# Optimization experiments

Measured on AMD Instinct MI355X. Metric: run time of the kernel, lower is better.

The kernel has to match this reference:

```python
import jax, jax.numpy as jnp
import numpy as np

B, N, M = 2, 2048, 2048
D = 1024          # query_dim == context_dim == inner_dim
H, DH = 16, 64    # heads, dim_head
SCALE = DH ** -0.5


def setup_inputs() -> dict:
    key = jax.random.key(0)
    ks = jax.random.split(key, 7)
    s = 0.02
    return {
        "x": jax.random.normal(ks[0], (B, N, D), jnp.float32),
        "context": jax.random.normal(ks[1], (B, M, D), jnp.float32),
        "Wq": jax.random.normal(ks[2], (D, H * DH), jnp.float32) * s,
        "Wk": jax.random.normal(ks[3], (D, H * DH), jnp.float32) * s,
        "Wv": jax.random.normal(ks[4], (D, H * DH), jnp.float32) * s,
        "Wo": jax.random.normal(ks[5], (H * DH, D), jnp.float32) * s,
        "bo": jax.random.normal(ks[6], (D,), jnp.float32) * s,
    }


def reference(x, context, Wq, Wk, Wv, Wo, bo):
    # Linear projections (bias-free, as in to_q/to_k/to_v)
    q = (x @ Wq).reshape(B, N, H, DH)        # [B,N,H,DH]
    k = (context @ Wk).reshape(B, M, H, DH)  # [B,M,H,DH]
    v = (context @ Wv).reshape(B, M, H, DH)
    # QK^T * scale, softmax over keys, then AV
    sim = jnp.einsum('bnhd,bmhd->bhnm', q, k) * SCALE  # [B,H,N,M]
    attn = jax.nn.softmax(sim, axis=-1)
    out = jnp.einsum('bhnm,bmhd->bnhd', attn, v)       # [B,N,H,DH]
    out = out.reshape(B, N, H * DH)
    return out @ Wo + bo  # to_out Linear; dropout=0 is identity
```

## Files before the change

### kernel.cpp

```cpp
#include <hip/hip_runtime.h>

#define B_  2
#define N_  2048
#define M_  2048
#define D_  1024
#define H_  16
#define DH_ 64

typedef __bf16 bf16x8 __attribute__((ext_vector_type(8)));
typedef __bf16 bf16x4 __attribute__((ext_vector_type(4)));
typedef short  short4v __attribute__((ext_vector_type(4)));
typedef float  f32x4  __attribute__((ext_vector_type(4)));
typedef unsigned int u32x4v __attribute__((ext_vector_type(4)));

#define GAS(p) ((__attribute__((address_space(1))) void*)(p))
#define LAS(p) ((__attribute__((address_space(3))) void*)(p))

#define QPRESCALE 0.18033688011112042f

__device__ __forceinline__ unsigned short f2bf(float f) {
    unsigned int u = __builtin_bit_cast(unsigned int, f);
    u += 0x7fffu + ((u >> 16) & 1u);
    return (unsigned short)(u >> 16);
}

__device__ __forceinline__ unsigned cvtpkbf(float a, float b) {
    unsigned r;
    asm("v_cvt_pk_bf16_f32 %0, %1, %2" : "=v"(r) : "v"(a), "v"(b));
    return r;
}

__global__ __launch_bounds__(256) void prep(
    const float* __restrict__ x, const float* __restrict__ ctx,
    const float* __restrict__ Wq, const float* __restrict__ Wk,
    const float* __restrict__ Wv, const float* __restrict__ Wo,
    unsigned short* __restrict__ xb, unsigned short* __restrict__ cb,
    unsigned short* __restrict__ WTbase)
{
    if (blockIdx.z == 4) {
        int blk = blockIdx.y * 32 + blockIdx.x;
        int stride = 1024 * 256;
        for (int i = blk * 256 + threadIdx.x; i < 2097152; i += stride) {
            const float4* src; unsigned short* dst; int j;
            if (i < 1048576) { src = (const float4*)x;   dst = xb; j = i; }
            else             { src = (const float4*)ctx; dst = cb; j = i - 1048576; }
            float4 v = src[j];
            ushort4 o = make_ushort4(f2bf(v.x), f2bf(v.y), f2bf(v.z), f2bf(v.w));
            *(ushort4*)(dst + 4*j) = o;
        }
        return;
    }
    const float* W = (blockIdx.z == 0) ? Wq : (blockIdx.z == 1) ? Wk
                    : (blockIdx.z == 2) ? Wv : Wo;
    unsigned short* WT = WTbase + (size_t)blockIdx.z * 1048576;
    __shared__ unsigned short t[32][33];
    int tx = threadIdx.x & 31, ty8 = threadIdx.x >> 5;
    int c = blockIdx.x * 32 + tx;
#pragma unroll
    for (int i = 0; i < 4; ++i) {
        int r = blockIdx.y * 32 + i*8 + ty8;
        t[i*8 + ty8][tx] = f2bf(W[(size_t)r * 1024 + c]);
    }
    __syncthreads();
    int c2 = blockIdx.y * 32 + tx;
#pragma unroll
    for (int i = 0; i < 4; ++i) {
        int r2 = blockIdx.x * 32 + i*8 + ty8;
        WT[(size_t)r2 * 1024 + c2] = t[tx][i*8 + ty8];
    }
}

__global__ __launch_bounds__(256) void gemm128(
    const unsigned short* __restrict__ xb,
    const unsigned short* __restrict__ cb,
    const unsigned short* __restrict__ wT,
    const unsigned short* __restrict__ aoA,
    unsigned short* __restrict__ qkv_out,
    const float* __restrict__ bo,
    float* __restrict__ outF,
    int base_mode)
{
    __shared__ __align__(16) unsigned short As[128*32];
    __shared__ __align__(16) unsigned short Bs[128*32];

    const int mode = base_mode + blockIdx.z;
    const unsigned short* Amat;
    const unsigned short* Bt;
    if (mode == 0)      { Amat = wT;               Bt = xb; }
    else if (mode == 1) { Amat = wT + 1048576;     Bt = cb; }
    else if (mode == 2) { Amat = cb;               Bt = wT + 2*1048576; }
    else                { Amat = wT + 3*1048576;   Bt = aoA; }

    const int tid = threadIdx.x;
    const int w = tid >> 6, l = tid & 63;
    const int quad = l >> 4, l16 = l & 15;
    const int wm = w & 1, wn = w >> 1;
    int row0, col0;
    if (mode == 2) { row0 = blockIdx.x * 128; col0 = blockIdx.y * 128; }
    else           { row0 = blockIdx.y * 128; col0 = blockIdx.x * 128; }

    f32x4 acc[4][4];
#pragma unroll
    for (int i = 0; i < 4; ++i)
#pragma unroll
        for (int j = 0; j < 4; ++j) acc[i][j] = (f32x4){0.f, 0.f, 0.f, 0.f};

    for (int k0 = 0; k0 < 1024; k0 += 32) {
        __syncthreads();
#pragma unroll
        for (int i = 0; i < 2; ++i) {
            int s = i*256 + w*64 + l;
            int m = s >> 2, c = s & 3;
            int cs = c ^ ((m >> 1) & 3);
            __builtin_amdgcn_global_load_lds(
                GAS(Amat + (size_t)(row0 + m)*1024 + k0 + cs*8),
                LAS(As + (i*256 + w*64)*8), 16, 0, 0);
            __builtin_amdgcn_global_load_lds(
                GAS(Bt + (size_t)(col0 + m)*1024 + k0 + cs*8),
                LAS(Bs + (i*256 + w*64)*8), 16, 0, 0);
        }
        __syncthreads();

        bf16x8 af[4], bfr[4];
#pragma unroll
        for (int mt = 0; mt < 4; ++mt) {
            int m = wm*64 + mt*16 + l16;
            af[mt] = *reinterpret_cast<const bf16x8*>(As + m*32 + (quad ^ ((m >> 1) & 3))*8);
            int n = wn*64 + mt*16 + l16;
            bfr[mt] = *reinterpret_cast<const bf16x8*>(Bs + n*32 + (quad ^ ((n >> 1) & 3))*8);
        }
#pragma unroll
        for (int mt = 0; mt < 4; ++mt)
#pragma unroll
            for (int nt = 0; nt < 4; ++nt)
                acc[mt][nt] = __builtin_amdgcn_mfma_f32_16x16x32_bf16(
                    af[mt], bfr[nt], acc[mt][nt], 0, 0, 0);
    }

    if (mode == 3) {
#pragma unroll
        for (int mt = 0; mt < 4; ++mt) {
            int c = row0 + wm*64 + mt*16 + quad*4;
            float4 bv = *(const float4*)(bo + c);
#pragma unroll
            for (int nt = 0; nt < 4; ++nt) {
                int n = col0 + wn*64 + nt*16 + l16;
                float4 ov = make_float4(acc[mt][nt][0] + bv.x, acc[mt][nt][1] + bv.y,
                                        acc[mt][nt][2] + bv.z, acc[mt][nt][3] + bv.w);
                *(float4*)(outF + (size_t)n*1024 + c) = ov;
            }
        }
    } else if (mode == 2) {
#pragma unroll
        for (int mt = 0; mt < 4; ++mt) {
            int gr = row0 + wm*64 + mt*16 + quad*4;
            int b = gr >> 11, nidx = gr & 2047;
#pragma unroll
            for (int nt = 0; nt < 4; ++nt) {
                int col = col0 + wn*64 + nt*16 + l16;
                int h = col >> 6, d = col & 63;
                ushort4 pk = make_ushort4(f2bf(acc[mt][nt][0]), f2bf(acc[mt][nt][1]),
                                          f2bf(acc[mt][nt][2]), f2bf(acc[mt][nt][3]));
                *(ushort4*)(qkv_out + (size_t)2*4194304
                            + (size_t)((b*16 + h)*64 + d)*2048 + nidx) = pk;
            }
        }
    } else {
        const float qs = (mode == 0) ? QPRESCALE : 1.0f;
        unsigned short* obase = qkv_out + (size_t)mode*4194304;
#pragma unroll
        for (int nt = 0; nt < 4; ++nt) {
            int n = col0 + wn*64 + nt*16 + l16;
            int b = n >> 11, nidx = n & 2047;
#pragma unroll
            for (int mt = 0; mt < 4; ++mt) {
                int c = row0 + wm*64 + mt*16 + quad*4;
                int h = c >> 6, d = c & 63;
                ushort4 pkv = make_ushort4(
                    f2bf(acc[mt][nt][0] * qs), f2bf(acc[mt][nt][1] * qs),
                    f2bf(acc[mt][nt][2] * qs), f2bf(acc[mt][nt][3] * qs));
                *(ushort4*)(obase + (size_t)((b*16 + h)*2048 + nidx)*64 + d) = pkv;
            }
        }
    }
}

__global__ __launch_bounds__(256, 2) void flash_attn(
    const unsigned short* __restrict__ qw,
    const unsigned short* __restrict__ kw,
    const unsigned short* __restrict__ vtw,
    unsigned short* __restrict__ ao)
{
    __shared__ __align__(16) unsigned short Tile[3][9216];

    const int tid = threadIdx.x;
    const int w = tid >> 6, l = tid & 63;
    const int quad = l >> 4, l16 = l & 15;
    const int bh = blockIdx.z * H_ + blockIdx.y;
    const int q0 = blockIdx.x * 128 + w * 32;

    int goff[5];
#pragma unroll
    for (int i = 0; i < 5; ++i) {
        int n = i*256 + w*64 + l;
        int m = (n < 576) ? n : n - 576;
        int row = m / 9, c = m % 9;  if (c > 7) c = 7;
        goff[i] = (n < 576) ? row*64 + c*8 : row*2048 + c*8;
    }
    const unsigned short* kbase = kw + (size_t)bh*131072;
    const unsigned short* vbase = vtw + (size_t)bh*131072;

    bf16x8 qf[2][2];
#pragma unroll
    for (int qg = 0; qg < 2; ++qg)
#pragma unroll
        for (int s = 0; s < 2; ++s)
            qf[qg][s] = *reinterpret_cast<const bf16x8*>(
                qw + (size_t)(bh*2048 + q0 + qg*16 + l16)*64 + s*32 + quad*8);

    f32x4 accO[2][4];
#pragma unroll
    for (int qg = 0; qg < 2; ++qg)
#pragma unroll
        for (int td = 0; td < 4; ++td) accO[qg][td] = (f32x4){0.f, 0.f, 0.f, 0.f};
    float lpart[2] = {0.f, 0.f};

    const f32x4 zz = (f32x4){0.f, 0.f, 0.f, 0.f};

    auto issue_tile = [&](int t, int b) {
        const unsigned short* kp = kbase + t*4096;
        const unsigned short* vp = vbase + t*64;
#pragma unroll
        for (int i = 0; i < 4; ++i) {
            const unsigned short* bp = (i*4 + w < 9) ? kp : vp;
            __builtin_amdgcn_global_load_lds(GAS(bp + goff[i]),
                LAS(&Tile[b][(i*256 + w*64)*8]), 16, 0, 0);
        }
        if (w < 2)
            __builtin_amdgcn_global_load_lds(GAS(vp + goff[4]),
                LAS(&Tile[b][(1024 + w*64)*8]), 16, 0, 0);
    };

    issue_tile(0, 0);
    issue_tile(1, 1);

    for (int it = 0; it < 32; ++it) {
        const int cur = it % 3;

        if (it < 31) {
            if (w < 2) asm volatile("s_waitcnt vmcnt(5)" ::: "memory");
            else       asm volatile("s_waitcnt vmcnt(4)" ::: "memory");
        } else {
            asm volatile("s_waitcnt vmcnt(0)" ::: "memory");
        }
        __builtin_amdgcn_s_barrier();

        if (it + 2 < 32) issue_tile(it + 2, (it + 2) % 3);

        const unsigned short* Ks = &Tile[cur][0];
        const unsigned short* Vs = &Tile[cur][4608];

        f32x4 sac[2][4];
        __builtin_amdgcn_s_setprio(1);
#pragma unroll
        for (int t = 0; t < 4; ++t) {
            const unsigned short* krow = Ks + (t*16 + l16)*72 + quad*8;
            bf16x8 kf0 = *reinterpret_cast<const bf16x8*>(krow);
            bf16x8 kf1 = *reinterpret_cast<const bf16x8*>(krow + 32);
            sac[0][t] = __builtin_amdgcn_mfma_f32_16x16x32_bf16(kf0, qf[0][0], zz, 0, 0, 0);
            sac[1][t] = __builtin_amdgcn_mfma_f32_16x16x32_bf16(kf0, qf[1][0], zz, 0, 0, 0);
            sac[0][t] = __builtin_amdgcn_mfma_f32_16x16x32_bf16(kf1, qf[0][1], sac[0][t], 0, 0, 0);
            sac[1][t] = __builtin_amdgcn_mfma_f32_16x16x32_bf16(kf1, qf[1][1], sac[1][t], 0, 0, 0);
        }
        __builtin_amdgcn_s_setprio(0);

        u32x4v pB[2][2];
#pragma unroll
        for (int qg = 0; qg < 2; ++qg) {
            float s0 = 0.f, s1 = 0.f, s2 = 0.f, s3 = 0.f;
#pragma unroll
            for (int t2 = 0; t2 < 2; ++t2) {
                float pe0 = __builtin_amdgcn_exp2f(sac[qg][2*t2][0]);
                float pe1 = __builtin_amdgcn_exp2f(sac[qg][2*t2][1]);
                float pe2 = __builtin_amdgcn_exp2f(sac[qg][2*t2][2]);
                float pe3 = __builtin_amdgcn_exp2f(sac[qg][2*t2][3]);
                float po0 = __builtin_amdgcn_exp2f(sac[qg][2*t2+1][0]);
                float po1 = __builtin_amdgcn_exp2f(sac[qg][2*t2+1][1]);
                float po2 = __builtin_amdgcn_exp2f(sac[qg][2*t2+1][2]);
                float po3 = __builtin_amdgcn_exp2f(sac[qg][2*t2+1][3]);
                s0 += pe0 + po0; s1 += pe1 + po1;
                s2 += pe2 + po2; s3 += pe3 + po3;
                unsigned b0 = cvtpkbf(pe0, pe1), b1 = cvtpkbf(pe2, pe3);
                unsigned b2 = cvtpkbf(po0, po1), b3 = cvtpkbf(po2, po3);
                asm("v_permlane32_swap_b32 %0, %1" : "+v"(b0), "+v"(b2));
                asm("v_permlane16_swap_b32 %0, %1" : "+v"(b0), "+v"(b2));
                asm("v_permlane32_swap_b32 %0, %1" : "+v"(b1), "+v"(b3));
                asm("v_permlane16_swap_b32 %0, %1" : "+v"(b1), "+v"(b3));
                pB[qg][t2] = (u32x4v){b0, b1, b2, b3};
            }
            lpart[qg] += (s0 + s1) + (s2 + s3);
        }

        __builtin_amdgcn_s_setprio(1);
#pragma unroll
        for (int td = 0; td < 4; ++td) {
            const unsigned short* vrow = Vs + (td*16 + l16)*72 + quad*8;
#pragma unroll
            for (int t2 = 0; t2 < 2; ++t2) {
                bf16x8 vf = *reinterpret_cast<const bf16x8*>(vrow + t2*32);
                accO[0][td] = __builtin_amdgcn_mfma_f32_16x16x32_bf16(
                    vf, __builtin_bit_cast(bf16x8, pB[0][t2]), accO[0][td], 0, 0, 0);
                accO[1][td] = __builtin_amdgcn_mfma_f32_16x16x32_bf16(
                    vf, __builtin_bit_cast(bf16x8, pB[1][t2]), accO[1][td], 0, 0, 0);
            }
        }
        __builtin_amdgcn_s_setprio(0);
    }

#pragma unroll
    for (int qg = 0; qg < 2; ++qg) {
        float s = lpart[qg];
        s += __shfl_xor(s, 16);
        s += __shfl_xor(s, 32);
        float inv = 1.f / s;
        const size_t rowbase =
            (size_t)(blockIdx.z*2048 + q0 + qg*16 + l16)*1024 + blockIdx.y*64;
#pragma unroll
        for (int td = 0; td < 4; ++td)
#pragma unroll
            for (int r = 0; r < 4; ++r)
                ao[rowbase + td*16 + quad*4 + r] = f2bf(accO[qg][td][r] * inv);
    }
}

extern "C" void kernel_launch(void* const* d_in, const int* in_sizes, int n_in,
                              void* d_out, int out_size, void* d_ws, size_t ws_size,
                              hipStream_t stream)
{
    const float* x   = (const float*)d_in[0];
    const float* ctx = (const float*)d_in[1];
    const float* Wq  = (const float*)d_in[2];
    const float* Wk  = (const float*)d_in[3];
    const float* Wv  = (const float*)d_in[4];
    const float* Wo  = (const float*)d_in[5];
    const float* bo  = (const float*)d_in[6];
    float* out = (float*)d_out;

    unsigned short* ws  = (unsigned short*)d_ws;
    unsigned short* xb  = ws;
    unsigned short* cb  = ws + 4194304;
    unsigned short* wT  = ws + 8388608;
    unsigned short* qkv = ws + 12582912;
    unsigned short* ao  = ws;

    prep<<<dim3(32, 32, 5), dim3(256), 0, stream>>>(x, ctx, Wq, Wk, Wv, Wo, xb, cb, wT);
    gemm128<<<dim3(32, 8, 3), dim3(256), 0, stream>>>(xb, cb, wT, ao, qkv, bo, out, 0);
    flash_attn<<<dim3(16, 16, 2), dim3(256), 0, stream>>>(qkv, qkv + 4194304, qkv + 8388608, ao);
    gemm128<<<dim3(32, 8, 1), dim3(256), 0, stream>>>(xb, cb, wT, ao, qkv, bo, out, 3);
}
```

Before: 203.4 us.

## Use 2 waves per flash-attention block with 64 query rows each

Flash attention blocks shrink from 4 waves to 2, each wave handling 64 query rows (four 16-row groups) instead of 32. Every K/V fragment read from LDS now feeds twice as many MFMAs, and the tile load is spread across 9 async global-to-LDS copies per thread with a single vmcnt wait. The cost is a much larger register footprint per wave (accumulators, scores, Q fragments) and fewer waves per block, which lowers the ability to hide latency. Launch bounds change to 128 threads with a minimum of 1 block per CU.

```diff
diff --git a/kernel.cpp b/kernel.cpp
--- a/kernel.cpp
+++ b/kernel.cpp
@@ -185,7 +185,7 @@
     }
 }
 
-__global__ __launch_bounds__(256, 2) void flash_attn(
+__global__ __launch_bounds__(128, 1) void flash_attn(
     const unsigned short* __restrict__ qw,
     const unsigned short* __restrict__ kw,
     const unsigned short* __restrict__ vtw,
@@ -197,12 +197,12 @@
     const int w = tid >> 6, l = tid & 63;
     const int quad = l >> 4, l16 = l & 15;
     const int bh = blockIdx.z * H_ + blockIdx.y;
-    const int q0 = blockIdx.x * 128 + w * 32;
-
-    int goff[5];
-#pragma unroll
-    for (int i = 0; i < 5; ++i) {
-        int n = i*256 + w*64 + l;
+    const int q0 = blockIdx.x * 128 + w * 64;
+
+    int goff[9];
+#pragma unroll
+    for (int i = 0; i < 9; ++i) {
+        int n = i*128 + w*64 + l;
         int m = (n < 576) ? n : n - 576;
         int row = m / 9, c = m % 9;  if (c > 7) c = 7;
         goff[i] = (n < 576) ? row*64 + c*8 : row*2048 + c*8;
@@ -210,20 +210,20 @@
     const unsigned short* kbase = kw + (size_t)bh*131072;
     const unsigned short* vbase = vtw + (size_t)bh*131072;
 
-    bf16x8 qf[2][2];
-#pragma unroll
-    for (int qg = 0; qg < 2; ++qg)
+    bf16x8 qf[4][2];
+#pragma unroll
+    for (int qg = 0; qg < 4; ++qg)
 #pragma unroll
         for (int s = 0; s < 2; ++s)
             qf[qg][s] = *reinterpret_cast<const bf16x8*>(
                 qw + (size_t)(bh*2048 + q0 + qg*16 + l16)*64 + s*32 + quad*8);
 
-    f32x4 accO[2][4];
-#pragma unroll
-    for (int qg = 0; qg < 2; ++qg)
+    f32x4 accO[4][4];
+#pragma unroll
+    for (int qg = 0; qg < 4; ++qg)
 #pragma unroll
         for (int td = 0; td < 4; ++td) accO[qg][td] = (f32x4){0.f, 0.f, 0.f, 0.f};
-    float lpart[2] = {0.f, 0.f};
+    float lpart[4] = {0.f, 0.f, 0.f, 0.f};
 
     const f32x4 zz = (f32x4){0.f, 0.f, 0.f, 0.f};
 
@@ -231,14 +231,14 @@
         const unsigned short* kp = kbase + t*4096;
         const unsigned short* vp = vbase + t*64;
 #pragma unroll
-        for (int i = 0; i < 4; ++i) {
-            const unsigned short* bp = (i*4 + w < 9) ? kp : vp;
+        for (int i = 0; i < 9; ++i) {
+            const unsigned short* bp = (i*128 + w*64 + 63 < 576) ? kp
+                                      : (i*128 + w*64 >= 576)    ? vp
+                                      : nullptr;
+            bp = ((i*128 + w*64) < 576) ? kp : vp;
             __builtin_amdgcn_global_load_lds(GAS(bp + goff[i]),
-                LAS(&Tile[b][(i*256 + w*64)*8]), 16, 0, 0);
-        }
-        if (w < 2)
-            __builtin_amdgcn_global_load_lds(GAS(vp + goff[4]),
-                LAS(&Tile[b][(1024 + w*64)*8]), 16, 0, 0);
+                LAS(&Tile[b][(i*128 + w*64)*8]), 16, 0, 0);
+        }
     };
 
     issue_tile(0, 0);
@@ -247,12 +247,8 @@
     for (int it = 0; it < 32; ++it) {
         const int cur = it % 3;
 
-        if (it < 31) {
-            if (w < 2) asm volatile("s_waitcnt vmcnt(5)" ::: "memory");
-            else       asm volatile("s_waitcnt vmcnt(4)" ::: "memory");
-        } else {
-            asm volatile("s_waitcnt vmcnt(0)" ::: "memory");
-        }
+        if (it < 31) asm volatile("s_waitcnt vmcnt(9)" ::: "memory");
+        else         asm volatile("s_waitcnt vmcnt(0)" ::: "memory");
         __builtin_amdgcn_s_barrier();
 
         if (it + 2 < 32) issue_tile(it + 2, (it + 2) % 3);
@@ -260,23 +256,24 @@
         const unsigned short* Ks = &Tile[cur][0];
         const unsigned short* Vs = &Tile[cur][4608];
 
-        f32x4 sac[2][4];
+        f32x4 sac[4][4];
         __builtin_amdgcn_s_setprio(1);
 #pragma unroll
         for (int t = 0; t < 4; ++t) {
             const unsigned short* krow = Ks + (t*16 + l16)*72 + quad*8;
             bf16x8 kf0 = *reinterpret_cast<const bf16x8*>(krow);
             bf16x8 kf1 = *reinterpret_cast<const bf16x8*>(krow + 32);
-            sac[0][t] = __builtin_amdgcn_mfma_f32_16x16x32_bf16(kf0, qf[0][0], zz, 0, 0, 0);
-            sac[1][t] = __builtin_amdgcn_mfma_f32_16x16x32_bf16(kf0, qf[1][0], zz, 0, 0, 0);
-            sac[0][t] = __builtin_amdgcn_mfma_f32_16x16x32_bf16(kf1, qf[0][1], sac[0][t], 0, 0, 0);
-            sac[1][t] = __builtin_amdgcn_mfma_f32_16x16x32_bf16(kf1, qf[1][1], sac[1][t], 0, 0, 0);
+#pragma unroll
+            for (int qg = 0; qg < 4; ++qg) {
+                sac[qg][t] = __builtin_amdgcn_mfma_f32_16x16x32_bf16(kf0, qf[qg][0], zz, 0, 0, 0);
+                sac[qg][t] = __builtin_amdgcn_mfma_f32_16x16x32_bf16(kf1, qf[qg][1], sac[qg][t], 0, 0, 0);
+            }
         }
         __builtin_amdgcn_s_setprio(0);
 
-        u32x4v pB[2][2];
-#pragma unroll
-        for (int qg = 0; qg < 2; ++qg) {
+        u32x4v pB[4][2];
+#pragma unroll
+        for (int qg = 0; qg < 4; ++qg) {
             float s0 = 0.f, s1 = 0.f, s2 = 0.f, s3 = 0.f;
 #pragma unroll
             for (int t2 = 0; t2 < 2; ++t2) {
@@ -305,20 +302,21 @@
 #pragma unroll
         for (int td = 0; td < 4; ++td) {
             const unsigned short* vrow = Vs + (td*16 + l16)*72 + quad*8;
-#pragma unroll
-            for (int t2 = 0; t2 < 2; ++t2) {
-                bf16x8 vf = *reinterpret_cast<const bf16x8*>(vrow + t2*32);
-                accO[0][td] = __builtin_amdgcn_mfma_f32_16x16x32_bf16(
-                    vf, __builtin_bit_cast(bf16x8, pB[0][t2]), accO[0][td], 0, 0, 0);
-                accO[1][td] = __builtin_amdgcn_mfma_f32_16x16x32_bf16(
-                    vf, __builtin_bit_cast(bf16x8, pB[1][t2]), accO[1][td], 0, 0, 0);
+            bf16x8 vf0 = *reinterpret_cast<const bf16x8*>(vrow);
+            bf16x8 vf1 = *reinterpret_cast<const bf16x8*>(vrow + 32);
+#pragma unroll
+            for (int qg = 0; qg < 4; ++qg) {
+                accO[qg][td] = __builtin_amdgcn_mfma_f32_16x16x32_bf16(
+                    vf0, __builtin_bit_cast(bf16x8, pB[qg][0]), accO[qg][td], 0, 0, 0);
+                accO[qg][td] = __builtin_amdgcn_mfma_f32_16x16x32_bf16(
+                    vf1, __builtin_bit_cast(bf16x8, pB[qg][1]), accO[qg][td], 0, 0, 0);
             }
         }
         __builtin_amdgcn_s_setprio(0);
     }
 
 #pragma unroll
-    for (int qg = 0; qg < 2; ++qg) {
+    for (int qg = 0; qg < 4; ++qg) {
         float s = lpart[qg];
         s += __shfl_xor(s, 16);
         s += __shfl_xor(s, 32);
@@ -355,6 +353,6 @@
 
     prep<<<dim3(32, 32, 5), dim3(256), 0, stream>>>(x, ctx, Wq, Wk, Wv, Wo, xb, cb, wT);
     gemm128<<<dim3(32, 8, 3), dim3(256), 0, stream>>>(xb, cb, wT, ao, qkv, bo, out, 0);
-    flash_attn<<<dim3(16, 16, 2), dim3(256), 0, stream>>>(qkv, qkv + 4194304, qkv + 8388608, ao);
+    flash_attn<<<dim3(16, 16, 2), dim3(128), 0, stream>>>(qkv, qkv + 4194304, qkv + 8388608, ao);
     gemm128<<<dim3(32, 8, 1), dim3(256), 0, stream>>>(xb, cb, wT, ao, qkv, bo, out, 3);
 }
```

New measurement: 212.8 us. +4.6%, slower.
